# Performance work log

Measured on AMD Instinct MI355X. Metric: run time of the kernel, lower is better.

## Reference

```python
import jax, jax.numpy as jnp
import numpy as np

BETA = 0.25  # commitment-loss weight (kwargs['beta'])


def setup_inputs() -> dict:
    key = jax.random.key(0)
    k1, k2 = jax.random.split(key)
    B, C, H, W = 16, 256, 64, 64
    K = 2048
    feats = jax.random.normal(k1, (B, C, H, W), dtype=jnp.float32)
    # nn.Embedding init: uniform(-1/n_codewords, 1/codeword_dim)
    codebook = jax.random.uniform(k2, (K, C), minval=-1.0 / K, maxval=1.0 / C,
                                  dtype=jnp.float32)
    return {"feats": feats, "codebook": codebook}


def reference(feats, codebook):
    B, C, H, W = feats.shape
    K = codebook.shape[0]
    z = jnp.transpose(feats, (0, 2, 3, 1))          # [B,H,W,C]
    zf = z.reshape(-1, C)                            # [N,C], N=B*H*W
    # squared-euclidean distances via ||z||^2 + ||e||^2 - 2 z.e : [N,K]
    d = (jnp.sum(zf * zf, axis=1, keepdims=True)
         + jnp.sum(codebook * codebook, axis=1)
         - 2.0 * (zf @ codebook.T))
    min_encoding_indices = jnp.argmin(d, axis=1)     # [N]
    mat_id_probs = jax.nn.softmax(-jnp.abs(d), axis=1)  # [N,K]
    z_q = codebook[min_encoding_indices].reshape(z.shape)  # [B,H,W,C]
    loss = (BETA * jnp.mean((jax.lax.stop_gradient(z_q) - z) ** 2)
            + jnp.mean((z_q - jax.lax.stop_gradient(z)) ** 2))
    # straight-through estimator
    z_q_st = z + jax.lax.stop_gradient(z_q - z)
    z_q_out = jnp.transpose(z_q_st, (0, 3, 1, 2))    # [B,C,H,W]
    idx_out = min_encoding_indices.reshape(B, H, W)
    probs_out = jnp.transpose(mat_id_probs.reshape(B, H, W, K), (0, 3, 1, 2))
    return z_q_out, idx_out, loss, probs_out
```

## Files before the change

### kernel.cpp

```cpp
#include <hip/hip_runtime.h>

#define HW 4096
#define CC 256
#define KK 2048
#define BB 16
#define NN (BB*HW)
#define RPB 128

#define ZQ_SZ   (BB*CC*HW)
#define IDX_OFF ZQ_SZ
#define LOSS_OFF (IDX_OFF + NN)
#define PROBS_OFF (LOSS_OFF + 1)

#define EH_OFF 0
#define EE_OFF 262144
#define EXT_OFF 264192
#define ZZ_OFF 280576
#define MS_OFF 346112
#define SS_OFF 477184
#define IKEY_OFF 608256

#define TAU 0.01f
#define CAND_CAP 512
#define KTC 32
#define KT_N 32
#define CS_N 17
#define HB 17408

typedef short bf16x8 __attribute__((ext_vector_type(8)));
typedef float f32x16 __attribute__((ext_vector_type(16)));
typedef unsigned int u32;
typedef unsigned long long u64;

__device__ __forceinline__ void gload16(const void* g, void* l){
  __builtin_amdgcn_global_load_lds(
      (const __attribute__((address_space(1))) u32*)g,
      (__attribute__((address_space(3))) u32*)l, 16, 0, 0);
}

__device__ __forceinline__ unsigned short bf16rn(float x){
  unsigned u = __float_as_uint(x);
  return (unsigned short)((u + 0x7fffu + ((u >> 16) & 1u)) >> 16);
}

#define PB(n0, n1) { \
  if (t < 64) asm volatile("s_waitcnt vmcnt(" n0 ")\n\ts_barrier" ::: "memory"); \
  else        asm volatile("s_waitcnt vmcnt(" n1 ")\n\ts_barrier" ::: "memory"); }

template<int STRIDE>
__device__ __forceinline__ float np_sumsq256(const float* __restrict__ a){
  float res0 = 0.f, res1 = 0.f;
  #pragma unroll
  for (int h = 0; h < 2; h++){
    const float* p = a + (size_t)h * 128 * STRIDE;
    float r[8];
    #pragma unroll
    for (int j = 0; j < 8; j++){ float x = p[(size_t)j * STRIDE]; r[j] = __fmul_rn(x, x); }
    for (int i = 8; i < 128; i += 8){
      #pragma unroll
      for (int j = 0; j < 8; j++){
        float x = p[(size_t)(i + j) * STRIDE];
        r[j] = __fadd_rn(r[j], __fmul_rn(x, x));
      }
    }
    float s = __fadd_rn(__fadd_rn(__fadd_rn(r[0], r[1]), __fadd_rn(r[2], r[3])),
                        __fadd_rn(__fadd_rn(r[4], r[5]), __fadd_rn(r[6], r[7])));
    if (h == 0) res0 = s; else res1 = s;
  }
  return __fadd_rn(res0, res1);
}

__global__ void k_cvt(const float* __restrict__ cb, float* __restrict__ out){
  const int i = blockIdx.x * 256 + threadIdx.x;
  const int k = i >> 5, c8 = (i & 31) * 8;
  const float* row = cb + (size_t)k * CC + c8;
  unsigned short v[8];
  #pragma unroll
  for (int j = 0; j < 8; ++j) v[j] = bf16rn(row[j]);
  *(uint4*)((unsigned short*)(out + EH_OFF) + (size_t)k * CC + c8) = *(uint4*)v;
}

__global__ void k_ee(const float* __restrict__ cb, float* __restrict__ out){
  const int k = blockIdx.x * 256 + threadIdx.x;
  unsigned short* ex = (unsigned short*)(out + EXT_OFF);
  float ee = np_sumsq256<1>(cb + (size_t)k * CC);
  out[EE_OFF + k] = ee;
  ex[k * 16] = bf16rn(-0.5f * ee);
  #pragma unroll
  for (int j = 1; j < 16; ++j) ex[k * 16 + j] = 0;
}

__global__ void k_zz(const float* __restrict__ feats, float* __restrict__ out){
  const int n = blockIdx.x * 256 + threadIdx.x;
  const int b = n >> 12, hw = n & 4095;
  out[ZZ_OFF + n] = np_sumsq256<HW>(feats + (size_t)b * CC * HW + hw);
}


#define GEMM_PROLOG \
  const int t = threadIdx.x; \
  const int w = t >> 6, l = t & 63; \
  const int grp = l >> 5; \
  const int lane31 = l & 31; \
  const int bid = blockIdx.x; \
  const int rb = bid >> 1, h = bid & 1; \
  const int n0 = rb * RPB; \
  const int bi = n0 >> 12; \
  const int hw0 = n0 & 4095; \
  const int myhw = hw0 + w * 32 + lane31; \
  bf16x8 ah0[16], ahx; \
  { \
    const float* zb = feats + (size_t)bi * CC * HW + myhw; \
    _Pragma("unroll") \
    for (int cs = 0; cs < 16; ++cs){ \
      _Pragma("unroll") \
      for (int j = 0; j < 8; ++j) \
        ah0[cs][j] = (short)bf16rn(zb[(size_t)(cs * 16 + grp * 8 + j) * HW]); \
    } \
    _Pragma("unroll") \
    for (int j = 0; j < 8; ++j) ahx[j] = 0; \
    if (grp == 0) ahx[0] = (short)0x3F80; \
  } \
  const unsigned short* ehg = (const unsigned short*)(out + EH_OFF) + (size_t)h * 1024 * CC; \
  const unsigned short* exg = (const unsigned short*)(out + EXT_OFF) + (size_t)h * 1024 * 16; \
  int ofs_[4]; \
  _Pragma("unroll") \
  for (int i = 0; i < 4; ++i){ \
    int ix = i * 256 + t; \
    int cd = ix & 31, g = (ix >> 5) & 1, cs = ix >> 6; \
    ofs_[i] = cd * CC + cs * 16 + g * 8; \
  } \
  int x_ofs = 0; \
  if (t < 64){ int cd = t & 31, g = (t >> 5) & 1; x_ofs = cd * 16 + g * 8; }

#define STAGE(KT, BI) { \
    unsigned char* bb_ = lds_e + (size_t)(BI) * HB; \
    const size_t kto_ = (size_t)(KT) * (KTC * CC); \
    _Pragma("unroll") \
    for (int i_ = 0; i_ < 4; ++i_) \
      gload16(ehg + ofs_[i_] + kto_, bb_ + (i_ * 256 + t) * 16); \
    if (t < 64) \
      gload16(exg + x_ofs + (size_t)(KT) * (KTC * 16), bb_ + (1024 + t) * 16); }

#define COMPUTE(BI) { \
    const unsigned char* hb_ = lds_e + (size_t)(BI) * HB; \
    _Pragma("unroll") \
    for (int ii = 0; ii < 16; ++ii){ accA[ii] = 0.f; accB[ii] = 0.f; } \
    _Pragma("unroll") \
    for (int cs = 0; cs < 16; ++cs){ \
      const unsigned char* bp_ = hb_ + (size_t)(cs * 2 + grp) * 512 + lane31 * 16; \
      bf16x8 e_ = *(const bf16x8*)(bp_); \
      if (cs & 1) accB = __builtin_amdgcn_mfma_f32_32x32x16_bf16(e_, ah0[cs], accB, 0, 0, 0); \
      else        accA = __builtin_amdgcn_mfma_f32_32x32x16_bf16(e_, ah0[cs], accA, 0, 0, 0); \
    } \
    { \
      const unsigned char* bp_ = hb_ + (size_t)(32 + grp) * 512 + lane31 * 16; \
      bf16x8 e_ = *(const bf16x8*)(bp_); \
      accA = __builtin_amdgcn_mfma_f32_32x32x16_bf16(e_, ahx, accA, 0, 0, 0); \
    } }

__global__ __launch_bounds__(256, 3)
void k_stats(const float* __restrict__ feats, float* __restrict__ out){
  __shared__ __align__(16) unsigned char lds_e[3 * HB];
  GEMM_PROLOG
  f32x16 accA, accB;
  float m0 = 3e38f, ss0 = 0.f;

  STAGE(0, 0);
  STAGE(1, 1);
  PB("5", "4")

  int cur = 0, nxt = 2;
  for (int kt = 0; kt < KT_N; ++kt){
    if (kt + 2 < KT_N) STAGE(kt + 2, nxt);
    COMPUTE(cur);
    #pragma unroll
    for (int r = 0; r < 16; ++r){
      float s = -2.f * (accA[r] + accB[r]);
      m0 = fminf(m0, s);
      ss0 += __expf(-s);
    }
    cur = cur == 2 ? 0 : cur + 1;
    nxt = nxt == 2 ? 0 : nxt + 1;
    if (kt == KT_N - 1) break;
    if (kt < KT_N - 2){ PB("5", "4") } else { PB("0", "0") }
  }
  m0 = fminf(m0, __shfl_xor(m0, 32));
  ss0 += __shfl_xor(ss0, 32);
  if (grp == 0){
    out[MS_OFF + h * NN + n0 + w * 32 + lane31] = m0;
    out[SS_OFF + h * NN + n0 + w * 32 + lane31] = ss0;
  }
}

__global__ __launch_bounds__(256, 2)
void k_probs(const float* __restrict__ feats, const float* __restrict__ cb,
             float* __restrict__ out){
  __shared__ __align__(16) unsigned char lds_e[3 * HB];
  __shared__ int cand[CAND_CAP];
  __shared__ int cand_n;
  GEMM_PROLOG
  if (t == 0) cand_n = 0;
  f32x16 accA, accB;

  const int myrow = n0 + w * 32 + lane31;
  float m0, inv0;
  {
    float ma = out[MS_OFF + myrow], mb = out[MS_OFF + NN + myrow];
    float sa = out[SS_OFF + myrow], sb = out[SS_OFF + NN + myrow];
    m0 = fminf(ma, mb);
    inv0 = 1.f / (sa + sb);
  }

  STAGE(0, 0);
  STAGE(1, 1);
  PB("5", "4")

  int cur = 0, nxt = 2;
  for (int kt = 0; kt < KT_N; ++kt){
    if (kt + 2 < KT_N) STAGE(kt + 2, nxt);
    COMPUTE(cur);
    float* pb = out + (size_t)PROBS_OFF
              + (size_t)(bi * KK + h * 1024 + kt * KTC + 4 * grp) * HW + myhw;
    #pragma unroll
    for (int r = 0; r < 16; ++r){
      int off = (r & 3) + 8 * (r >> 2);
      float s = -2.f * (accA[r] + accB[r]);
      pb[(size_t)off * HW] = __expf(-s) * inv0;
      if (s <= m0 + TAU){
        int sl = atomicAdd(&cand_n, 1);
        if (sl < CAND_CAP)
          cand[sl] = ((w * 32 + lane31) << 16) | (h * 1024 + kt * KTC + 4 * grp + off);
      }
    }
    cur = cur == 2 ? 0 : cur + 1;
    nxt = nxt == 2 ? 0 : nxt + 1;
    if (kt == KT_N - 1) break;
    if (kt == 0)            { PB("21", "20") }
    else if (kt < KT_N - 2) { PB("37", "36") }
    else                    { PB("16", "16") }
  }
  __syncthreads();

  u64* ikey = (u64*)(out + IKEY_OFF);
  int nc = cand_n; if (nc > CAND_CAP) nc = CAND_CAP;
  for (int i = t; i < nc; i += 256){
    int rc = cand[i];
    int rl = (rc >> 16) & 127, code = rc & 2047;
    int n = n0 + rl;
    const float* zp = feats + (size_t)(n >> 12) * CC * HW + (n & 4095);
    const float* ep = cb + (size_t)code * CC;
    float a = 0.f;
    #pragma unroll 8
    for (int c = 0; c < CC; ++c) a = __builtin_fmaf(zp[(size_t)c * HW], ep[c], a);
    float t1 = __fadd_rn(out[ZZ_OFF + n], out[EE_OFF + code]);
    float d = __fadd_rn(t1, -2.f * a);
    u64 key = ((u64)__float_as_uint(d) << 32) | (unsigned)code;
    atomicMin(&ikey[n], key);
  }
}

__global__ void k_final(const float* __restrict__ feats, const float* __restrict__ cb,
                        float* __restrict__ out){
  const int t = threadIdx.x;
  const int n = blockIdx.x * 256 + t;
  const u64* ikey = (const u64*)(out + IKEY_OFF);
  int code = (int)(ikey[n] & 2047u);
  out[IDX_OFF + n] = (float)code;
  const int bi = n >> 12, hw = n & 4095;
  const float* ep = cb + (size_t)code * CC;
  const float* zp = feats + (size_t)bi * CC * HW + hw;
  float s = 0.f;
  for (int c = 0; c < CC; ++c){
    float dz = ep[c] - zp[(size_t)c * HW];
    s = __builtin_fmaf(dz, dz, s);
  }
  #pragma unroll
  for (int off = 32; off; off >>= 1) s += __shfl_xor(s, off);
  if ((t & 63) == 0) atomicAdd(out + LOSS_OFF, s * (1.25f / 16777216.f));
}

__global__ void k_zq(const float* __restrict__ cb, float* __restrict__ out){
  const int f4 = blockIdx.x * 256 + threadIdx.x;
  const int f = f4 * 4;
  const int b = f >> 20;
  const int rem = f & 1048575;
  const int c = rem >> 12;
  const int hw = rem & 4095;
  const int n = b * HW + hw;
  const float* idxf = out + IDX_OFF;
  float4 iv = *(const float4*)(idxf + n);
  float4 o;
  o.x = cb[(size_t)((int)iv.x) * CC + c];
  o.y = cb[(size_t)((int)iv.y) * CC + c];
  o.z = cb[(size_t)((int)iv.z) * CC + c];
  o.w = cb[(size_t)((int)iv.w) * CC + c];
  *(float4*)(out + f) = o;
}

extern "C" void kernel_launch(void* const* d_in, const int* in_sizes, int n_in,
                              void* d_out, int out_size, void* d_ws, size_t ws_size,
                              hipStream_t stream){
  const float* feats = (const float*)d_in[0];
  const float* cb    = (const float*)d_in[1];
  float* out = (float*)d_out;

  (void)hipMemsetAsync(out + LOSS_OFF, 0, sizeof(float), stream);
  (void)hipMemsetAsync(out + IKEY_OFF, 0xFF, (size_t)NN * 8, stream);
  hipLaunchKernelGGL(k_cvt,   dim3(256),   dim3(256), 0, stream, cb, out);
  hipLaunchKernelGGL(k_ee,    dim3(8),     dim3(256), 0, stream, cb, out);
  hipLaunchKernelGGL(k_zz,    dim3(256),   dim3(256), 0, stream, feats, out);
  hipLaunchKernelGGL(k_stats, dim3(1024),  dim3(256), 0, stream, feats, out);
  hipLaunchKernelGGL(k_probs, dim3(1024),  dim3(256), 0, stream, feats, cb, out);
  hipLaunchKernelGGL(k_final, dim3(256),   dim3(256), 0, stream, feats, cb, out);
  hipLaunchKernelGGL(k_zq,    dim3(16384), dim3(256), 0, stream, cb, out);
}
```

Measured before the change: 517.5 us.

## Double rows per block in distance GEMMs and drop separate zz kernel

Each wave now computes two 32-row tiles against every staged codebook tile, so RPB goes from 128 to 256 and the grid halves. This reuses each LDS codebook fragment for twice as many MFMAs and halves codebook staging traffic. The per-row ||z||^2 kernel is removed and recomputed on the fly only for argmin candidates inside k_probs. The cost is higher register pressure (occupancy bound lowered to 2 in k_stats), fewer blocks to fill the CUs, and retuned barrier wait counts.

```diff
diff --git a/kernel.cpp b/kernel.cpp
--- a/kernel.cpp
+++ b/kernel.cpp
@@ -5,7 +5,7 @@
 #define KK 2048
 #define BB 16
 #define NN (BB*HW)
-#define RPB 128
+#define RPB 256
 
 #define ZQ_SZ   (BB*CC*HW)
 #define IDX_OFF ZQ_SZ
@@ -15,7 +15,6 @@
 #define EH_OFF 0
 #define EE_OFF 262144
 #define EXT_OFF 264192
-#define ZZ_OFF 280576
 #define MS_OFF 346112
 #define SS_OFF 477184
 #define IKEY_OFF 608256
@@ -24,7 +23,6 @@
 #define CAND_CAP 512
 #define KTC 32
 #define KT_N 32
-#define CS_N 17
 #define HB 17408
 
 typedef short bf16x8 __attribute__((ext_vector_type(8)));
@@ -90,12 +88,6 @@
   for (int j = 1; j < 16; ++j) ex[k * 16 + j] = 0;
 }
 
-__global__ void k_zz(const float* __restrict__ feats, float* __restrict__ out){
-  const int n = blockIdx.x * 256 + threadIdx.x;
-  const int b = n >> 12, hw = n & 4095;
-  out[ZZ_OFF + n] = np_sumsq256<HW>(feats + (size_t)b * CC * HW + hw);
-}
-
 
 #define GEMM_PROLOG \
   const int t = threadIdx.x; \
@@ -107,15 +99,18 @@
   const int n0 = rb * RPB; \
   const int bi = n0 >> 12; \
   const int hw0 = n0 & 4095; \
-  const int myhw = hw0 + w * 32 + lane31; \
-  bf16x8 ah0[16], ahx; \
+  const int hwA = hw0 + w * 64 + lane31; \
+  bf16x8 ahA[16], ahB[16], ahx; \
   { \
-    const float* zb = feats + (size_t)bi * CC * HW + myhw; \
+    const float* zb = feats + (size_t)bi * CC * HW + hwA; \
     _Pragma("unroll") \
     for (int cs = 0; cs < 16; ++cs){ \
       _Pragma("unroll") \
-      for (int j = 0; j < 8; ++j) \
-        ah0[cs][j] = (short)bf16rn(zb[(size_t)(cs * 16 + grp * 8 + j) * HW]); \
+      for (int j = 0; j < 8; ++j){ \
+        size_t co = (size_t)(cs * 16 + grp * 8 + j) * HW; \
+        ahA[cs][j] = (short)bf16rn(zb[co]); \
+        ahB[cs][j] = (short)bf16rn(zb[co + 32]); \
+      } \
     } \
     _Pragma("unroll") \
     for (int j = 0; j < 8; ++j) ahx[j] = 0; \
@@ -145,26 +140,32 @@
 #define COMPUTE(BI) { \
     const unsigned char* hb_ = lds_e + (size_t)(BI) * HB; \
     _Pragma("unroll") \
-    for (int ii = 0; ii < 16; ++ii){ accA[ii] = 0.f; accB[ii] = 0.f; } \
+    for (int ii = 0; ii < 16; ++ii){ a00[ii]=0.f; a01[ii]=0.f; a10[ii]=0.f; a11[ii]=0.f; } \
     _Pragma("unroll") \
     for (int cs = 0; cs < 16; ++cs){ \
       const unsigned char* bp_ = hb_ + (size_t)(cs * 2 + grp) * 512 + lane31 * 16; \
       bf16x8 e_ = *(const bf16x8*)(bp_); \
-      if (cs & 1) accB = __builtin_amdgcn_mfma_f32_32x32x16_bf16(e_, ah0[cs], accB, 0, 0, 0); \
-      else        accA = __builtin_amdgcn_mfma_f32_32x32x16_bf16(e_, ah0[cs], accA, 0, 0, 0); \
+      if (cs & 1){ \
+        a01 = __builtin_amdgcn_mfma_f32_32x32x16_bf16(e_, ahA[cs], a01, 0, 0, 0); \
+        a11 = __builtin_amdgcn_mfma_f32_32x32x16_bf16(e_, ahB[cs], a11, 0, 0, 0); \
+      } else { \
+        a00 = __builtin_amdgcn_mfma_f32_32x32x16_bf16(e_, ahA[cs], a00, 0, 0, 0); \
+        a10 = __builtin_amdgcn_mfma_f32_32x32x16_bf16(e_, ahB[cs], a10, 0, 0, 0); \
+      } \
     } \
     { \
       const unsigned char* bp_ = hb_ + (size_t)(32 + grp) * 512 + lane31 * 16; \
       bf16x8 e_ = *(const bf16x8*)(bp_); \
-      accA = __builtin_amdgcn_mfma_f32_32x32x16_bf16(e_, ahx, accA, 0, 0, 0); \
+      a00 = __builtin_amdgcn_mfma_f32_32x32x16_bf16(e_, ahx, a00, 0, 0, 0); \
+      a10 = __builtin_amdgcn_mfma_f32_32x32x16_bf16(e_, ahx, a10, 0, 0, 0); \
     } }
 
-__global__ __launch_bounds__(256, 3)
+__global__ __launch_bounds__(256, 2)
 void k_stats(const float* __restrict__ feats, float* __restrict__ out){
   __shared__ __align__(16) unsigned char lds_e[3 * HB];
   GEMM_PROLOG
-  f32x16 accA, accB;
-  float m0 = 3e38f, ss0 = 0.f;
+  f32x16 a00, a01, a10, a11;
+  float mA = 3e38f, sA = 0.f, mB = 3e38f, sB = 0.f;
 
   STAGE(0, 0);
   STAGE(1, 1);
@@ -176,20 +177,24 @@
     COMPUTE(cur);
     #pragma unroll
     for (int r = 0; r < 16; ++r){
-      float s = -2.f * (accA[r] + accB[r]);
-      m0 = fminf(m0, s);
-      ss0 += __expf(-s);
+      float s0 = -2.f * (a00[r] + a01[r]);
+      float s1 = -2.f * (a10[r] + a11[r]);
+      mA = fminf(mA, s0); sA += __expf(-s0);
+      mB = fminf(mB, s1); sB += __expf(-s1);
     }
     cur = cur == 2 ? 0 : cur + 1;
     nxt = nxt == 2 ? 0 : nxt + 1;
     if (kt == KT_N - 1) break;
     if (kt < KT_N - 2){ PB("5", "4") } else { PB("0", "0") }
   }
-  m0 = fminf(m0, __shfl_xor(m0, 32));
-  ss0 += __shfl_xor(ss0, 32);
+  mA = fminf(mA, __shfl_xor(mA, 32)); sA += __shfl_xor(sA, 32);
+  mB = fminf(mB, __shfl_xor(mB, 32)); sB += __shfl_xor(sB, 32);
   if (grp == 0){
-    out[MS_OFF + h * NN + n0 + w * 32 + lane31] = m0;
-    out[SS_OFF + h * NN + n0 + w * 32 + lane31] = ss0;
+    int r0 = n0 + w * 64 + lane31;
+    out[MS_OFF + h * NN + r0]      = mA;
+    out[SS_OFF + h * NN + r0]      = sA;
+    out[MS_OFF + h * NN + r0 + 32] = mB;
+    out[SS_OFF + h * NN + r0 + 32] = sB;
   }
 }
 
@@ -201,15 +206,17 @@
   __shared__ int cand_n;
   GEMM_PROLOG
   if (t == 0) cand_n = 0;
-  f32x16 accA, accB;
-
-  const int myrow = n0 + w * 32 + lane31;
-  float m0, inv0;
+  f32x16 a00, a01, a10, a11;
+
+  const int myrowA = n0 + w * 64 + lane31;
+  float m0A, inv0A, m0B, inv0B;
   {
-    float ma = out[MS_OFF + myrow], mb = out[MS_OFF + NN + myrow];
-    float sa = out[SS_OFF + myrow], sb = out[SS_OFF + NN + myrow];
-    m0 = fminf(ma, mb);
-    inv0 = 1.f / (sa + sb);
+    float ma = out[MS_OFF + myrowA], mb = out[MS_OFF + NN + myrowA];
+    float sa = out[SS_OFF + myrowA], sb = out[SS_OFF + NN + myrowA];
+    m0A = fminf(ma, mb); inv0A = 1.f / (sa + sb);
+    ma = out[MS_OFF + myrowA + 32]; mb = out[MS_OFF + NN + myrowA + 32];
+    sa = out[SS_OFF + myrowA + 32]; sb = out[SS_OFF + NN + myrowA + 32];
+    m0B = fminf(ma, mb); inv0B = 1.f / (sa + sb);
   }
 
   STAGE(0, 0);
@@ -221,24 +228,29 @@
     if (kt + 2 < KT_N) STAGE(kt + 2, nxt);
     COMPUTE(cur);
     float* pb = out + (size_t)PROBS_OFF
-              + (size_t)(bi * KK + h * 1024 + kt * KTC + 4 * grp) * HW + myhw;
+              + (size_t)(bi * KK + h * 1024 + kt * KTC + 4 * grp) * HW + hwA;
     #pragma unroll
     for (int r = 0; r < 16; ++r){
       int off = (r & 3) + 8 * (r >> 2);
-      float s = -2.f * (accA[r] + accB[r]);
-      pb[(size_t)off * HW] = __expf(-s) * inv0;
-      if (s <= m0 + TAU){
+      float s0 = -2.f * (a00[r] + a01[r]);
+      float s1 = -2.f * (a10[r] + a11[r]);
+      float* p = pb + (size_t)off * HW;
+      p[0]  = __expf(-s0) * inv0A;
+      p[32] = __expf(-s1) * inv0B;
+      int cg = h * 1024 + kt * KTC + 4 * grp + off;
+      if (s0 <= m0A + TAU){
         int sl = atomicAdd(&cand_n, 1);
-        if (sl < CAND_CAP)
-          cand[sl] = ((w * 32 + lane31) << 16) | (h * 1024 + kt * KTC + 4 * grp + off);
+        if (sl < CAND_CAP) cand[sl] = ((w * 64 + lane31) << 16) | cg;
+      }
+      if (s1 <= m0B + TAU){
+        int sl = atomicAdd(&cand_n, 1);
+        if (sl < CAND_CAP) cand[sl] = ((w * 64 + 32 + lane31) << 16) | cg;
       }
     }
     cur = cur == 2 ? 0 : cur + 1;
     nxt = nxt == 2 ? 0 : nxt + 1;
     if (kt == KT_N - 1) break;
-    if (kt == 0)            { PB("21", "20") }
-    else if (kt < KT_N - 2) { PB("37", "36") }
-    else                    { PB("16", "16") }
+    if (kt == 0){ PB("37", "36") } else { PB("63", "63") }
   }
   __syncthreads();
 
@@ -246,14 +258,15 @@
   int nc = cand_n; if (nc > CAND_CAP) nc = CAND_CAP;
   for (int i = t; i < nc; i += 256){
     int rc = cand[i];
-    int rl = (rc >> 16) & 127, code = rc & 2047;
+    int rl = (rc >> 16) & 255, code = rc & 2047;
     int n = n0 + rl;
     const float* zp = feats + (size_t)(n >> 12) * CC * HW + (n & 4095);
     const float* ep = cb + (size_t)code * CC;
     float a = 0.f;
     #pragma unroll 8
     for (int c = 0; c < CC; ++c) a = __builtin_fmaf(zp[(size_t)c * HW], ep[c], a);
-    float t1 = __fadd_rn(out[ZZ_OFF + n], out[EE_OFF + code]);
+    float zzv = np_sumsq256<HW>(zp);
+    float t1 = __fadd_rn(zzv, out[EE_OFF + code]);
     float d = __fadd_rn(t1, -2.f * a);
     u64 key = ((u64)__float_as_uint(d) << 32) | (unsigned)code;
     atomicMin(&ikey[n], key);
@@ -309,9 +322,8 @@
   (void)hipMemsetAsync(out + IKEY_OFF, 0xFF, (size_t)NN * 8, stream);
   hipLaunchKernelGGL(k_cvt,   dim3(256),   dim3(256), 0, stream, cb, out);
   hipLaunchKernelGGL(k_ee,    dim3(8),     dim3(256), 0, stream, cb, out);
-  hipLaunchKernelGGL(k_zz,    dim3(256),   dim3(256), 0, stream, feats, out);
-  hipLaunchKernelGGL(k_stats, dim3(1024),  dim3(256), 0, stream, feats, out);
-  hipLaunchKernelGGL(k_probs, dim3(1024),  dim3(256), 0, stream, feats, cb, out);
+  hipLaunchKernelGGL(k_stats, dim3(512),   dim3(256), 0, stream, feats, out);
+  hipLaunchKernelGGL(k_probs, dim3(512),   dim3(256), 0, stream, feats, cb, out);
   hipLaunchKernelGGL(k_final, dim3(256),   dim3(256), 0, stream, feats, cb, out);
   hipLaunchKernelGGL(k_zq,    dim3(16384), dim3(256), 0, stream, cb, out);
 }
```

After: 517.2 us. About the same (-0.1%).
